# Kernel optimization log

Hardware: AMD Instinct MI355X
Metric: run time of the kernel (lower is better)

Reference implementation:

```python
import jax, jax.numpy as jnp
import numpy as np

E = 8        # n_routed_experts
K = 2        # n_experts_per_token
H = 1024     # d_hidden
D = 512      # d_expert
NSH = 2      # n_shared_experts -> shared expert width = D*NSH


def setup_inputs() -> dict:
    key = jax.random.key(0)
    ks = jax.random.split(key, 8)
    s = 0.02
    x = jax.random.normal(ks[0], (4, 2048, H), jnp.float32)
    W_router = (jax.random.normal(ks[1], (H, E), jnp.float32) * s)
    Wg = (jax.random.normal(ks[2], (E, H, D), jnp.float32) * s)   # per-expert gate proj
    Wu = (jax.random.normal(ks[3], (E, H, D), jnp.float32) * s)   # per-expert up proj
    Wd = (jax.random.normal(ks[4], (E, D, H), jnp.float32) * s)   # per-expert down proj
    Ds = D * NSH
    Wsg = (jax.random.normal(ks[5], (H, Ds), jnp.float32) * s)
    Wsu = (jax.random.normal(ks[6], (H, Ds), jnp.float32) * s)
    Wsd = (jax.random.normal(ks[7], (Ds, H), jnp.float32) * s)
    return {"x": x, "W_router": W_router, "Wg": Wg, "Wu": Wu, "Wd": Wd,
            "Wsg": Wsg, "Wsu": Wsu, "Wsd": Wsd}


def reference(x, W_router, Wg, Wu, Wd, Wsg, Wsu, Wsd):
    B, S, Hd = x.shape
    T = B * S
    xf = x.reshape(T, Hd)

    # shared expert (SwiGLU)
    shared = (jax.nn.silu(xf @ Wsg) * (xf @ Wsu)) @ Wsd          # [T, H]

    # gating: softmax -> top-k -> renormalize
    logits = xf @ W_router                                        # [T, E]
    probs = jax.nn.softmax(logits, axis=-1)
    topk_scores, topk_idx = jax.lax.top_k(probs, K)               # [T, K]
    topk_scores = topk_scores / jnp.sum(topk_scores, axis=-1, keepdims=True)

    # combine weights: zero for unselected experts (topk indices are distinct,
    # so the original's first-match score selection equals a simple scatter)
    combine = jnp.zeros((T, E), x.dtype).at[jnp.arange(T)[:, None], topk_idx].set(topk_scores)

    # per-expert SwiGLU, computed densely and combined with sparse weights
    gate = jax.nn.silu(jnp.einsum('th,ehd->etd', xf, Wg))         # [E, T, D]
    up = jnp.einsum('th,ehd->etd', xf, Wu)                        # [E, T, D]
    expert_out = jnp.einsum('etd,edh->eth', gate * up, Wd)        # [E, T, H]
    routed = jnp.einsum('eth,te->th', expert_out, combine)        # [T, H]

    out = (routed + shared).reshape(B, S, Hd)

    # load-balancing aux loss: E * sum(mean_probs^2)
    probs_mean = jnp.mean(probs.reshape(B, S, E), axis=(0, 1))
    aux_loss = E * jnp.sum(probs_mean * probs_mean)
    return out, aux_loss
```

## Files before the change

kernel.cpp:

```cpp
#include <hip/hip_runtime.h>


typedef unsigned short u16;
typedef unsigned int   u32;
typedef short short8 __attribute__((ext_vector_type(8)));
typedef float f32x4  __attribute__((ext_vector_type(4)));

#define AS1 __attribute__((address_space(1)))
#define AS3 __attribute__((address_space(3)))

constexpr int T  = 8192;
constexpr int H  = 1024;
constexpr int E  = 8;
constexpr int D  = 512;
constexpr int DS = 1024;
constexpr int PAIR_CAP  = 18432;
constexpr int MT_ROUTED = 72;
constexpr int RB = 512;

constexpr int GU_ROUTED_BLKS = 4 * MT_ROUTED;
constexpr int GU_SHARED_BLKS = 8 * (T / 256);
constexpr int DR_BLKS = 4 * MT_ROUTED;
constexpr int DSH_BLKS = 4 * (T / 256);

__device__ __forceinline__ u16 f2bf(float f){
  u32 u = __builtin_bit_cast(u32, f);
  u += 0x7fffu + ((u >> 16) & 1u);
  return (u16)(u >> 16);
}
__device__ __forceinline__ float bf2f(u16 h){
  u32 u = ((u32)h) << 16;
  return __builtin_bit_cast(float, u);
}

__device__ __forceinline__ void gl_lds16(const u16* g, u16* l){
  __builtin_amdgcn_global_load_lds((const AS1 void*)g, (AS3 void*)l, 16, 0, 0);
}

__device__ __forceinline__ void wait_vmcnt4(){ __builtin_amdgcn_s_waitcnt(0x0f74); }
__device__ __forceinline__ void wait_vmcnt0(){ __builtin_amdgcn_s_waitcnt(0x0f70); }

__device__ __forceinline__ void bar(){
  __builtin_amdgcn_s_barrier();
  __builtin_amdgcn_sched_barrier(0);
}

__device__ __forceinline__ int swz_off(int c, int lane){
  return ((c ^ (lane & 7)) * 8);
}

__global__ void __launch_bounds__(256) router_kernel(
    const float* __restrict__ x, const float* __restrict__ Wr,
    u16* __restrict__ xb,
    int* __restrict__ topk_idx, float* __restrict__ topk_w,
    int* __restrict__ partial_hist, float* __restrict__ partial_probs)
{
  __shared__ int   hist_s[4][8];
  __shared__ float ps_s[4][8];
  int tid = threadIdx.x, lane = tid & 63, wv = tid >> 6;
  int   histl[8] = {0,0,0,0,0,0,0,0};
  float psl[8]   = {0.f,0.f,0.f,0.f,0.f,0.f,0.f,0.f};

  for (int it = 0; it < 4; ++it){
    int t = blockIdx.x * 16 + wv * 4 + it;
    const float4* xr = (const float4*)(x + (long)t * H);
    uint2* xbr = (uint2*)(xb + (long)t * H);
    float acc[8];
#pragma unroll
    for (int e = 0; e < 8; ++e) acc[e] = 0.f;
#pragma unroll
    for (int i = 0; i < 4; ++i){
      float4 xv = xr[i * 64 + lane];
      u32 lo = (u32)f2bf(xv.x) | ((u32)f2bf(xv.y) << 16);
      u32 hi = (u32)f2bf(xv.z) | ((u32)f2bf(xv.w) << 16);
      xbr[i * 64 + lane] = make_uint2(lo, hi);
      int h0 = i * 256 + lane * 4;
#pragma unroll
      for (int j = 0; j < 4; ++j){
        float xs = (j == 0) ? xv.x : (j == 1) ? xv.y : (j == 2) ? xv.z : xv.w;
        const float4* wr = (const float4*)(Wr + (long)(h0 + j) * E);
        float4 w0 = wr[0], w1 = wr[1];
        acc[0] += xs * w0.x; acc[1] += xs * w0.y; acc[2] += xs * w0.z; acc[3] += xs * w0.w;
        acc[4] += xs * w1.x; acc[5] += xs * w1.y; acc[6] += xs * w1.z; acc[7] += xs * w1.w;
      }
    }
#pragma unroll
    for (int off = 32; off >= 1; off >>= 1){
#pragma unroll
      for (int e = 0; e < 8; ++e) acc[e] += __shfl_xor(acc[e], off, 64);
    }
    if (lane == 0){
      float m = acc[0];
#pragma unroll
      for (int e = 1; e < 8; ++e) m = fmaxf(m, acc[e]);
      float p[8], s = 0.f;
#pragma unroll
      for (int e = 0; e < 8; ++e){ p[e] = __expf(acc[e] - m); s += p[e]; }
      float inv = 1.f / s;
#pragma unroll
      for (int e = 0; e < 8; ++e) psl[e] += p[e] * inv;
      int i1 = 0; float v1 = p[0];
#pragma unroll
      for (int e = 1; e < 8; ++e) if (p[e] > v1){ v1 = p[e]; i1 = e; }
      int i2 = -1; float v2 = -1.f;
#pragma unroll
      for (int e = 0; e < 8; ++e) if (e != i1 && p[e] > v2){ v2 = p[e]; i2 = e; }
      float rs = 1.f / (v1 + v2);
      topk_idx[2 * t] = i1; topk_idx[2 * t + 1] = i2;
      topk_w[2 * t] = v1 * rs; topk_w[2 * t + 1] = v2 * rs;
      histl[i1]++; histl[i2]++;
    }
  }
  if (lane == 0){
#pragma unroll
    for (int e = 0; e < 8; ++e){ hist_s[wv][e] = histl[e]; ps_s[wv][e] = psl[e]; }
  }
  __syncthreads();
  if (tid < 8){
    int hs = 0; float ps = 0.f;
#pragma unroll
    for (int w = 0; w < 4; ++w){ hs += hist_s[w][tid]; ps += ps_s[w][tid]; }
    partial_hist[blockIdx.x * 8 + tid]  = hs;
    partial_probs[blockIdx.x * 8 + tid] = ps;
  }
}

__global__ void __launch_bounds__(64) scan_kernel(
    const int* __restrict__ partial_hist, const float* __restrict__ partial_probs,
    int* __restrict__ block_offset, float* __restrict__ out_aux,
    int* __restrict__ meta)
{
  __shared__ int   csum[8][8];
  __shared__ float cps[8][8];
  __shared__ int   cbase[8][8];
  __shared__ int   base_s[8];
  int tid = threadIdx.x, e = tid & 7, c = tid >> 3;
  int s = 0; float f = 0.f;
  for (int b = c * 64; b < c * 64 + 64; ++b){
    s += partial_hist[b * 8 + e]; f += partial_probs[b * 8 + e];
  }
  csum[c][e] = s; cps[c][e] = f;
  __syncthreads();
  if (tid < 8){
    int tot = 0;
    for (int cc = 0; cc < 8; ++cc){ cbase[cc][tid] = tot; tot += csum[cc][tid]; }
    csum[0][tid] = tot;
  }
  __syncthreads();
  if (tid == 0){
    int off = 0;
    for (int ee = 0; ee < 8; ++ee){ base_s[ee] = off; off += (csum[0][ee] + 255) & ~255; }
    meta[0] = off;
    float a = 0.f;
    for (int ee = 0; ee < 8; ++ee){
      float ps = 0.f;
      for (int cc = 0; cc < 8; ++cc) ps += cps[cc][ee];
      float m = ps * (1.f / (float)T);
      a += m * m;
    }
    out_aux[0] = (float)E * a;
  }
  __syncthreads();
  int run = base_s[e] + cbase[c][e];
  for (int b = c * 64; b < c * 64 + 64; ++b){
    block_offset[b * 8 + e] = run;
    run += partial_hist[b * 8 + e];
  }
}

__global__ void __launch_bounds__(64) scatter_kernel(
    const int* __restrict__ topk_idx, const float* __restrict__ topk_w,
    const int* __restrict__ block_offset,
    int* __restrict__ pair_token, int* __restrict__ pair_expert,
    float* __restrict__ pair_score, int* __restrict__ token_pos)
{
  int lane = threadIdx.x, b = blockIdx.x;
  if (lane >= 32) return;
  int idx = b * 32 + lane;
  int t = idx >> 1;
  int e = topk_idx[idx];
  float w = topk_w[idx];
  unsigned long long below = lane ? ((1ull << lane) - 1ull) : 0ull;
  int rank = 0, basee = 0;
#pragma unroll
  for (int ee = 0; ee < 8; ++ee){
    unsigned long long m = __ballot(e == ee);
    if (e == ee){ rank = __popcll(m & below); basee = block_offset[b * 8 + ee]; }
  }
  int pos = basee + rank;
  pair_token[pos] = t;
  pair_expert[pos] = e;
  pair_score[pos] = w;
  token_pos[idx] = pos;
}

__global__ void __launch_bounds__(256) transpose_all(
    const float* __restrict__ Wsg, const float* __restrict__ Wsu, u16* __restrict__ WsguT,
    const float* __restrict__ Wsd, u16* __restrict__ WsdT,
    const float* __restrict__ Wg,  const float* __restrict__ Wu, u16* __restrict__ WguT,
    const float* __restrict__ Wd,  u16* __restrict__ WdT)
{
  __shared__ float tile[32][33];
  int z = blockIdx.z;
  const float* src; u16* dst; int R, C, itype;
  if (z < 3){
    R = 1024; C = 1024;
    if (z == 0){ src = Wsg; dst = WsguT; itype = 1; }
    else if (z == 1){ src = Wsu; dst = WsguT; itype = 2; }
    else { src = Wsd; dst = WsdT; itype = 0; }
  } else if (z < 19){
    R = 1024; C = 512;
    int p = z - 3;
    if (p < 8){ src = Wg + (long)p * R * C; dst = WguT + (long)p * (2 * D * H); itype = 1; }
    else      { src = Wu + (long)(p - 8) * R * C; dst = WguT + (long)(p - 8) * (2 * D * H); itype = 2; }
  } else {
    R = 512; C = 1024;
    int p = z - 19;
    src = Wd + (long)p * R * C; dst = WdT + (long)p * R * C; itype = 0;
  }
  int tx = threadIdx.x & 31, ty = threadIdx.x >> 5;
  int c = blockIdx.x * 32 + tx;
  int rb = blockIdx.y * 32;
  if (blockIdx.x * 32 >= C || rb >= R) return;
#pragma unroll
  for (int j = 0; j < 4; ++j)
    tile[ty + j * 8][tx] = src[(long)(rb + ty + j * 8) * C + c];
  __syncthreads();
#pragma unroll
  for (int j = 0; j < 4; ++j){
    int cc = blockIdx.x * 32 + ty + j * 8;
    int dr = (itype == 0) ? cc : ((cc >> 4) * 32 + (cc & 15) + ((itype == 2) ? 16 : 0));
    dst[(long)dr * R + rb + tx] = f2bf(tile[tx][ty + j * 8]);
  }
}

struct HalfStage { const u16* p[2]; };

__device__ __forceinline__ void half_init(HalfStage& hs, const u16* __restrict__ gbase,
    int ld, int rowbase, const int* __restrict__ gather, int wave, int lane){
  int lr = lane >> 3, ch = lane & 7;
  int chs = (ch ^ lr) * 8;
#pragma unroll
  for (int j = 0; j < 2; ++j){
    int row = (wave * 2 + j) * 8 + lr;
    int grow = gather ? gather[rowbase + row] : (rowbase + row);
    hs.p[j] = gbase + (long)grow * ld + chs;
  }
}

__device__ __forceinline__ void half_issue(const HalfStage& hs, int k0,
                                           u16* __restrict__ lds, int wave){
#pragma unroll
  for (int j = 0; j < 2; ++j)
    gl_lds16(hs.p[j] + k0, lds + (wave * 2 + j) * 512);
}

template<int EPI>
__device__ __forceinline__ void gemm256(
    const u16* __restrict__ A, const u16* __restrict__ B, int K, int NT,
    const int* __restrict__ gather, int m0, int n0,
    u16* __restrict__ o_bf, int o_ld,
    const float* __restrict__ pair_score,
    const int* __restrict__ token_pos, const u16* __restrict__ rout,
    float* __restrict__ out,
    u16* __restrict__ As, u16* __restrict__ Bs)
{
  int tid = threadIdx.x, lane = tid & 63, wave = tid >> 6;
  int wm = wave >> 2, wn = wave & 3;
  int rl = lane & 15, q = lane >> 4;

  HalfStage a0, a1, b0, b1;
  half_init(a0, A, K, m0,       gather, wave, lane);
  half_init(a1, A, K, m0 + 128, gather, wave, lane);
  half_init(b0, B, K, n0,       nullptr, wave, lane);
  half_init(b1, B, K, n0 + 128, nullptr, wave, lane);

  f32x4 acc[8][4];
#pragma unroll
  for (int i = 0; i < 8; ++i)
#pragma unroll
    for (int j = 0; j < 4; ++j)
#pragma unroll
      for (int r = 0; r < 4; ++r) acc[i][j][r] = 0.f;

  half_issue(b0, 0, Bs + 0 * 8192, wave);
  half_issue(b1, 0, Bs + 1 * 8192, wave);
  half_issue(a0, 0, As + 0 * 8192, wave);
  half_issue(a1, 0, As + 1 * 8192, wave);
  if (NT > 1){
    half_issue(b0, 64, Bs + 2 * 8192, wave);
    half_issue(b1, 64, Bs + 3 * 8192, wave);
    wait_vmcnt4();
  } else {
    wait_vmcnt0();
  }
  bar();

  int bhalf = wn >> 1, brow0 = (wn & 1) * 64;

#pragma unroll 1
  for (int t = 0; t < NT; ++t){
    int buf = t & 1, nbuf = buf ^ 1;
    const u16* Abase = As + (buf * 2 + wm) * 8192;
    const u16* Bbase = Bs + (buf * 2 + bhalf) * 8192;
    short8 bfr[2][4];
#pragma unroll
    for (int qd = 0; qd < 4; ++qd){
      short8 afr[2][2];
#pragma unroll
      for (int ks = 0; ks < 2; ++ks){
        int off = swz_off(ks * 4 + q, lane);
#pragma unroll
        for (int m = 0; m < 2; ++m)
          afr[ks][m] = *(const short8*)(Abase + (qd * 32 + m * 16 + rl) * 64 + off);
        if (qd == 0){
#pragma unroll
          for (int n = 0; n < 4; ++n)
            bfr[ks][n] = *(const short8*)(Bbase + (brow0 + n * 16 + rl) * 64 + off);
        }
      }
      if (qd == 0 && t + 1 < NT) half_issue(a0, (t + 1) * 64, As + (nbuf * 2 + 0) * 8192, wave);
      if (qd == 1 && t + 1 < NT) half_issue(a1, (t + 1) * 64, As + (nbuf * 2 + 1) * 8192, wave);
      if (qd == 2 && t + 2 < NT) half_issue(b0, (t + 2) * 64, Bs + (buf * 2 + 0) * 8192, wave);
      if (qd == 3 && t + 2 < NT) half_issue(b1, (t + 2) * 64, Bs + (buf * 2 + 1) * 8192, wave);
      bar();
      __builtin_amdgcn_s_setprio(1);
#pragma unroll
      for (int ks = 0; ks < 2; ++ks)
#pragma unroll
        for (int m = 0; m < 2; ++m)
#pragma unroll
          for (int n = 0; n < 4; ++n)
            acc[qd * 2 + m][n] = __builtin_amdgcn_mfma_f32_16x16x32_bf16(
                afr[ks][m], bfr[ks][n], acc[qd * 2 + m][n], 0, 0, 0);
      __builtin_amdgcn_s_setprio(0);
      if (qd == 3){
        if (t + 2 < NT) wait_vmcnt4(); else wait_vmcnt0();
      }
      bar();
    }
  }

  int row0 = m0 + wm * 128;
  if constexpr (EPI == 0){
    int hcol0 = (n0 >> 1) + wn * 32;
#pragma unroll
    for (int mt = 0; mt < 8; ++mt)
#pragma unroll
      for (int ntp = 0; ntp < 2; ++ntp)
#pragma unroll
        for (int r = 0; r < 4; ++r){
          int row = row0 + mt * 16 + q * 4 + r;
          int col = hcol0 + ntp * 16 + rl;
          float g = acc[mt][2 * ntp][r], u = acc[mt][2 * ntp + 1][r];
          float h = g / (1.f + __expf(-g)) * u;
          o_bf[(long)row * o_ld + col] = f2bf(h);
        }
  } else if constexpr (EPI == 1){
    int col0 = n0 + wn * 64;
#pragma unroll
    for (int mt = 0; mt < 8; ++mt)
#pragma unroll
      for (int r = 0; r < 4; ++r){
        int row = row0 + mt * 16 + q * 4 + r;
        float s = pair_score[row];
        long rbase = (long)row * H;
#pragma unroll
        for (int n = 0; n < 4; ++n){
          int col = col0 + n * 16 + rl;
          o_bf[rbase + col] = f2bf(s * acc[mt][n][r]);
        }
      }
  } else {
    int col0 = n0 + wn * 64;
#pragma unroll
    for (int mt = 0; mt < 8; ++mt)
#pragma unroll
      for (int r = 0; r < 4; ++r){
        int row = row0 + mt * 16 + q * 4 + r;
        int p0 = token_pos[2 * row], p1 = token_pos[2 * row + 1];
        long o = (long)row * H;
#pragma unroll
        for (int n = 0; n < 4; ++n){
          int col = col0 + n * 16 + rl;
          out[o + col] = acc[mt][n][r]
                       + bf2f(rout[(long)p0 * H + col])
                       + bf2f(rout[(long)p1 * H + col]);
        }
      }
  }
}

__global__ void __launch_bounds__(512, 2) gateup_fused(
    const u16* __restrict__ xb, const u16* __restrict__ WguT, u16* __restrict__ hr,
    const u16* __restrict__ WsguT, u16* __restrict__ hs,
    const int* __restrict__ pair_token, const int* __restrict__ pair_expert,
    const int* __restrict__ meta)
{
  __shared__ u16 As[4 * 8192];
  __shared__ u16 Bs[4 * 8192];
  int fid = blockIdx.x;
  if (fid < GU_ROUTED_BLKS){
    int x8 = fid & 7, s = fid >> 3;
    int mtile = x8 + 8 * (s >> 2), ntile = s & 3;
    int m0 = mtile * 256;
    if (m0 >= meta[0]) return;
    int e = pair_expert[m0];
    gemm256<0>(xb, WguT + (long)e * (2 * D * H), H, H / 64, pair_token,
               m0, ntile * 256, hr, D, nullptr, nullptr, nullptr, nullptr, As, Bs);
  } else {
    int lid = fid - GU_ROUTED_BLKS;
    int x8 = lid & 7, s = lid >> 3;
    int mtile = x8 + 8 * (s >> 3), ntile = s & 7;
    gemm256<0>(xb, WsguT, H, H / 64, nullptr,
               mtile * 256, ntile * 256, hs, DS, nullptr, nullptr, nullptr, nullptr, As, Bs);
  }
}

__global__ void __launch_bounds__(512, 2) down_routed_kernel(
    const u16* __restrict__ hr, const u16* __restrict__ WdT, u16* __restrict__ rout,
    const float* __restrict__ pair_score, const int* __restrict__ pair_expert,
    const int* __restrict__ meta)
{
  __shared__ u16 As[4 * 8192];
  __shared__ u16 Bs[4 * 8192];
  int fid = blockIdx.x;
  int x8 = fid & 7, s = fid >> 3;
  int mtile = x8 + 8 * (s >> 2), ntile = s & 3;
  int m0 = mtile * 256;
  if (m0 >= meta[0]) return;
  int e = pair_expert[m0];
  gemm256<1>(hr, WdT + (long)e * (H * D), D, D / 64, nullptr,
             m0, ntile * 256, rout, H, pair_score, nullptr, nullptr, nullptr, As, Bs);
}

__global__ void __launch_bounds__(512, 2) down_shared_kernel(
    const u16* __restrict__ hs, const u16* __restrict__ WsdT,
    const u16* __restrict__ rout, const int* __restrict__ token_pos,
    float* __restrict__ out)
{
  __shared__ u16 As[4 * 8192];
  __shared__ u16 Bs[4 * 8192];
  int fid = blockIdx.x;
  int x8 = fid & 7, s = fid >> 3;
  int mtile = x8 + 8 * (s >> 2), ntile = s & 3;
  gemm256<2>(hs, WsdT, DS, DS / 64, nullptr,
             mtile * 256, ntile * 256, nullptr, 0, nullptr, token_pos, rout, out, As, Bs);
}

extern "C" void kernel_launch(void* const* d_in, const int* in_sizes, int n_in,
                              void* d_out, int out_size, void* d_ws, size_t ws_size,
                              hipStream_t stream)
{
  (void)in_sizes; (void)n_in; (void)out_size; (void)ws_size;
  const float* x   = (const float*)d_in[0];
  const float* Wr  = (const float*)d_in[1];
  const float* Wg  = (const float*)d_in[2];
  const float* Wu  = (const float*)d_in[3];
  const float* Wd  = (const float*)d_in[4];
  const float* Wsg = (const float*)d_in[5];
  const float* Wsu = (const float*)d_in[6];
  const float* Wsd = (const float*)d_in[7];
  float* out = (float*)d_out;

  char* ws = (char*)d_ws;
  size_t off = 0;
  auto alloc = [&](size_t bytes) -> void* {
    void* p = ws + off; off += (bytes + 255) & ~(size_t)255; return p;
  };
  u16* xb    = (u16*)alloc((size_t)T * H * 2);
  u16* WsguT = (u16*)alloc((size_t)2 * DS * H * 2);
  u16* WsdT  = (u16*)alloc((size_t)H * DS * 2);
  u16* WguT  = (u16*)alloc((size_t)E * 2 * D * H * 2);
  u16* WdT   = (u16*)alloc((size_t)E * H * D * 2);
  u16* hs    = (u16*)alloc((size_t)T * DS * 2);
  u16* hr    = (u16*)alloc((size_t)PAIR_CAP * D * 2);
  u16* rout  = (u16*)alloc((size_t)PAIR_CAP * H * 2);
  int*   topk_idx  = (int*)alloc((size_t)T * 2 * 4);
  float* topk_w    = (float*)alloc((size_t)T * 2 * 4);
  int*   token_pos = (int*)alloc((size_t)T * 2 * 4);
  int*   partial_hist  = (int*)alloc((size_t)RB * 8 * 4);
  float* partial_probs = (float*)alloc((size_t)RB * 8 * 4);
  int*   block_offset  = (int*)alloc((size_t)RB * 8 * 4);
  int*   meta          = (int*)alloc(256);
  char* zbase = ws + off;
  int*   pair_token  = (int*)alloc((size_t)PAIR_CAP * 4);
  int*   pair_expert = (int*)alloc((size_t)PAIR_CAP * 4);
  float* pair_score  = (float*)alloc((size_t)PAIR_CAP * 4);
  size_t zbytes = (size_t)((ws + off) - zbase);

  hipMemsetAsync(zbase, 0, zbytes, stream);

  transpose_all<<<dim3(32, 32, 27), 256, 0, stream>>>(
      Wsg, Wsu, WsguT, Wsd, WsdT, Wg, Wu, WguT, Wd, WdT);

  router_kernel<<<RB, 256, 0, stream>>>(x, Wr, xb, topk_idx, topk_w,
                                        partial_hist, partial_probs);
  scan_kernel<<<1, 64, 0, stream>>>(partial_hist, partial_probs, block_offset,
                                    out + (size_t)T * H, meta);
  scatter_kernel<<<RB, 64, 0, stream>>>(topk_idx, topk_w, block_offset,
                                        pair_token, pair_expert, pair_score, token_pos);

  gateup_fused<<<GU_ROUTED_BLKS + GU_SHARED_BLKS, 512, 0, stream>>>(
      xb, WguT, hr, WsguT, hs, pair_token, pair_expert, meta);

  down_routed_kernel<<<DR_BLKS, 512, 0, stream>>>(
      hr, WdT, rout, pair_score, pair_expert, meta);
  down_shared_kernel<<<DSH_BLKS, 512, 0, stream>>>(
      hs, WsdT, rout, token_pos, out);
}
```

Measured before the change: 364.0 us.

## Halve down-proj N tile, double block count, add XCD-aware block remapping

Templates the GEMM on the number of B halves so the down-projection kernels use 256x128 tiles instead of 256x256, doubling their grid size and halving their B LDS buffers. This targets low occupancy and wave quantization in the down-projection kernels. It also replaces the old interleaved tile mapping with an XCD-aware block index permutation in all three GEMM kernels, aiming for better L2 reuse per chiplet. A sched_barrier is also added before the s_barrier. The cost is more re-reads of the A operand because there are more N tiles.

Result: faster. 354.5 us (-2.6%).

```diff
diff --git a/kernel.cpp b/kernel.cpp
--- a/kernel.cpp
+++ b/kernel.cpp
@@ -20,8 +20,9 @@
 
 constexpr int GU_ROUTED_BLKS = 4 * MT_ROUTED;
 constexpr int GU_SHARED_BLKS = 8 * (T / 256);
-constexpr int DR_BLKS = 4 * MT_ROUTED;
-constexpr int DSH_BLKS = 4 * (T / 256);
+constexpr int GU_BLKS  = GU_ROUTED_BLKS + GU_SHARED_BLKS;
+constexpr int DR_BLKS  = 8 * MT_ROUTED;
+constexpr int DSH_BLKS = 8 * (T / 256);
 
 __device__ __forceinline__ u16 f2bf(float f){
   u32 u = __builtin_bit_cast(u32, f);
@@ -37,16 +38,22 @@
   __builtin_amdgcn_global_load_lds((const AS1 void*)g, (AS3 void*)l, 16, 0, 0);
 }
 
-__device__ __forceinline__ void wait_vmcnt4(){ __builtin_amdgcn_s_waitcnt(0x0f74); }
-__device__ __forceinline__ void wait_vmcnt0(){ __builtin_amdgcn_s_waitcnt(0x0f70); }
+template<int N>
+__device__ __forceinline__ void wait_vm(){ __builtin_amdgcn_s_waitcnt(0x0f70 | N); }
 
 __device__ __forceinline__ void bar(){
+  __builtin_amdgcn_sched_barrier(0);
   __builtin_amdgcn_s_barrier();
   __builtin_amdgcn_sched_barrier(0);
 }
 
 __device__ __forceinline__ int swz_off(int c, int lane){
   return ((c ^ (lane & 7)) * 8);
+}
+
+template<int NWG>
+__device__ __forceinline__ int xcd_tau(int fid){
+  return (fid & 7) * (NWG >> 3) + (fid >> 3);
 }
 
 __global__ void __launch_bounds__(256) router_kernel(
@@ -255,7 +262,7 @@
     gl_lds16(hs.p[j] + k0, lds + (wave * 2 + j) * 512);
 }
 
-template<int EPI>
+template<int EPI, int BH>
 __device__ __forceinline__ void gemm256(
     const u16* __restrict__ A, const u16* __restrict__ B, int K, int NT,
     const int* __restrict__ gather, int m0, int n0,
@@ -265,6 +272,7 @@
     float* __restrict__ out,
     u16* __restrict__ As, u16* __restrict__ Bs)
 {
+  constexpr int NB = 2 * BH;
   int tid = threadIdx.x, lane = tid & 63, wave = tid >> 6;
   int wm = wave >> 2, wn = wave & 3;
   int rl = lane & 15, q = lane >> 4;
@@ -273,37 +281,38 @@
   half_init(a0, A, K, m0,       gather, wave, lane);
   half_init(a1, A, K, m0 + 128, gather, wave, lane);
   half_init(b0, B, K, n0,       nullptr, wave, lane);
-  half_init(b1, B, K, n0 + 128, nullptr, wave, lane);
-
-  f32x4 acc[8][4];
+  if (BH == 2) half_init(b1, B, K, n0 + 128, nullptr, wave, lane);
+
+  f32x4 acc[8][NB];
 #pragma unroll
   for (int i = 0; i < 8; ++i)
 #pragma unroll
-    for (int j = 0; j < 4; ++j)
+    for (int j = 0; j < NB; ++j)
 #pragma unroll
       for (int r = 0; r < 4; ++r) acc[i][j][r] = 0.f;
 
   half_issue(b0, 0, Bs + 0 * 8192, wave);
-  half_issue(b1, 0, Bs + 1 * 8192, wave);
+  if (BH == 2) half_issue(b1, 0, Bs + 1 * 8192, wave);
   half_issue(a0, 0, As + 0 * 8192, wave);
   half_issue(a1, 0, As + 1 * 8192, wave);
   if (NT > 1){
-    half_issue(b0, 64, Bs + 2 * 8192, wave);
-    half_issue(b1, 64, Bs + 3 * 8192, wave);
-    wait_vmcnt4();
+    half_issue(b0, 64, Bs + (BH + 0) * 8192, wave);
+    if (BH == 2) half_issue(b1, 64, Bs + 3 * 8192, wave);
+    wait_vm<2 * BH>();
   } else {
-    wait_vmcnt0();
+    wait_vm<0>();
   }
   bar();
 
-  int bhalf = wn >> 1, brow0 = (wn & 1) * 64;
+  int bhalf = (BH == 2) ? (wn >> 1) : 0;
+  int brow0 = (BH == 2) ? (wn & 1) * 64 : wn * 32;
 
 #pragma unroll 1
   for (int t = 0; t < NT; ++t){
     int buf = t & 1, nbuf = buf ^ 1;
     const u16* Abase = As + (buf * 2 + wm) * 8192;
-    const u16* Bbase = Bs + (buf * 2 + bhalf) * 8192;
-    short8 bfr[2][4];
+    const u16* Bbase = Bs + (buf * BH + bhalf) * 8192;
+    short8 bfr[2][NB];
 #pragma unroll
     for (int qd = 0; qd < 4; ++qd){
       short8 afr[2][2];
@@ -315,14 +324,14 @@
           afr[ks][m] = *(const short8*)(Abase + (qd * 32 + m * 16 + rl) * 64 + off);
         if (qd == 0){
 #pragma unroll
-          for (int n = 0; n < 4; ++n)
+          for (int n = 0; n < NB; ++n)
             bfr[ks][n] = *(const short8*)(Bbase + (brow0 + n * 16 + rl) * 64 + off);
         }
       }
       if (qd == 0 && t + 1 < NT) half_issue(a0, (t + 1) * 64, As + (nbuf * 2 + 0) * 8192, wave);
       if (qd == 1 && t + 1 < NT) half_issue(a1, (t + 1) * 64, As + (nbuf * 2 + 1) * 8192, wave);
-      if (qd == 2 && t + 2 < NT) half_issue(b0, (t + 2) * 64, Bs + (buf * 2 + 0) * 8192, wave);
-      if (qd == 3 && t + 2 < NT) half_issue(b1, (t + 2) * 64, Bs + (buf * 2 + 1) * 8192, wave);
+      if (qd == 2 && t + 2 < NT) half_issue(b0, (t + 2) * 64, Bs + (buf * BH + 0) * 8192, wave);
+      if (BH == 2 && qd == 3 && t + 2 < NT) half_issue(b1, (t + 2) * 64, Bs + (buf * 2 + 1) * 8192, wave);
       bar();
       __builtin_amdgcn_s_setprio(1);
 #pragma unroll
@@ -330,12 +339,12 @@
 #pragma unroll
         for (int m = 0; m < 2; ++m)
 #pragma unroll
-          for (int n = 0; n < 4; ++n)
+          for (int n = 0; n < NB; ++n)
             acc[qd * 2 + m][n] = __builtin_amdgcn_mfma_f32_16x16x32_bf16(
                 afr[ks][m], bfr[ks][n], acc[qd * 2 + m][n], 0, 0, 0);
       __builtin_amdgcn_s_setprio(0);
       if (qd == 3){
-        if (t + 2 < NT) wait_vmcnt4(); else wait_vmcnt0();
+        if (t + 2 < NT) wait_vm<2 * BH>(); else wait_vm<0>();
       }
       bar();
     }
@@ -357,7 +366,7 @@
           o_bf[(long)row * o_ld + col] = f2bf(h);
         }
   } else if constexpr (EPI == 1){
-    int col0 = n0 + wn * 64;
+    int col0 = n0 + wn * (16 * NB);
 #pragma unroll
     for (int mt = 0; mt < 8; ++mt)
 #pragma unroll
@@ -366,13 +375,13 @@
         float s = pair_score[row];
         long rbase = (long)row * H;
 #pragma unroll
-        for (int n = 0; n < 4; ++n){
+        for (int n = 0; n < NB; ++n){
           int col = col0 + n * 16 + rl;
           o_bf[rbase + col] = f2bf(s * acc[mt][n][r]);
         }
       }
   } else {
-    int col0 = n0 + wn * 64;
+    int col0 = n0 + wn * (16 * NB);
 #pragma unroll
     for (int mt = 0; mt < 8; ++mt)
 #pragma unroll
@@ -381,7 +390,7 @@
         int p0 = token_pos[2 * row], p1 = token_pos[2 * row + 1];
         long o = (long)row * H;
 #pragma unroll
-        for (int n = 0; n < 4; ++n){
+        for (int n = 0; n < NB; ++n){
           int col = col0 + n * 16 + rl;
           out[o + col] = acc[mt][n][r]
                        + bf2f(rout[(long)p0 * H + col])
@@ -399,21 +408,19 @@
 {
   __shared__ u16 As[4 * 8192];
   __shared__ u16 Bs[4 * 8192];
-  int fid = blockIdx.x;
-  if (fid < GU_ROUTED_BLKS){
-    int x8 = fid & 7, s = fid >> 3;
-    int mtile = x8 + 8 * (s >> 2), ntile = s & 3;
+  int tau = xcd_tau<GU_BLKS>(blockIdx.x);
+  if (tau < GU_ROUTED_BLKS){
+    int mtile = tau >> 2, ntile = tau & 3;
     int m0 = mtile * 256;
     if (m0 >= meta[0]) return;
     int e = pair_expert[m0];
-    gemm256<0>(xb, WguT + (long)e * (2 * D * H), H, H / 64, pair_token,
-               m0, ntile * 256, hr, D, nullptr, nullptr, nullptr, nullptr, As, Bs);
+    gemm256<0, 2>(xb, WguT + (long)e * (2 * D * H), H, H / 64, pair_token,
+                  m0, ntile * 256, hr, D, nullptr, nullptr, nullptr, nullptr, As, Bs);
   } else {
-    int lid = fid - GU_ROUTED_BLKS;
-    int x8 = lid & 7, s = lid >> 3;
-    int mtile = x8 + 8 * (s >> 3), ntile = s & 7;
-    gemm256<0>(xb, WsguT, H, H / 64, nullptr,
-               mtile * 256, ntile * 256, hs, DS, nullptr, nullptr, nullptr, nullptr, As, Bs);
+    int sidx = tau - GU_ROUTED_BLKS;
+    int mtile = sidx >> 3, ntile = sidx & 7;
+    gemm256<0, 2>(xb, WsguT, H, H / 64, nullptr,
+                  mtile * 256, ntile * 256, hs, DS, nullptr, nullptr, nullptr, nullptr, As, Bs);
   }
 }
 
@@ -423,15 +430,14 @@
     const int* __restrict__ meta)
 {
   __shared__ u16 As[4 * 8192];
-  __shared__ u16 Bs[4 * 8192];
-  int fid = blockIdx.x;
-  int x8 = fid & 7, s = fid >> 3;
-  int mtile = x8 + 8 * (s >> 2), ntile = s & 3;
+  __shared__ u16 Bs[2 * 8192];
+  int tau = xcd_tau<DR_BLKS>(blockIdx.x);
+  int mtile = tau >> 3, ntile = tau & 7;
   int m0 = mtile * 256;
   if (m0 >= meta[0]) return;
   int e = pair_expert[m0];
-  gemm256<1>(hr, WdT + (long)e * (H * D), D, D / 64, nullptr,
-             m0, ntile * 256, rout, H, pair_score, nullptr, nullptr, nullptr, As, Bs);
+  gemm256<1, 1>(hr, WdT + (long)e * (H * D), D, D / 64, nullptr,
+                m0, ntile * 128, rout, H, pair_score, nullptr, nullptr, nullptr, As, Bs);
 }
 
 __global__ void __launch_bounds__(512, 2) down_shared_kernel(
@@ -440,12 +446,11 @@
     float* __restrict__ out)
 {
   __shared__ u16 As[4 * 8192];
-  __shared__ u16 Bs[4 * 8192];
-  int fid = blockIdx.x;
-  int x8 = fid & 7, s = fid >> 3;
-  int mtile = x8 + 8 * (s >> 2), ntile = s & 3;
-  gemm256<2>(hs, WsdT, DS, DS / 64, nullptr,
-             mtile * 256, ntile * 256, nullptr, 0, nullptr, token_pos, rout, out, As, Bs);
+  __shared__ u16 Bs[2 * 8192];
+  int tau = xcd_tau<DSH_BLKS>(blockIdx.x);
+  int mtile = tau >> 3, ntile = tau & 7;
+  gemm256<2, 1>(hs, WsdT, DS, DS / 64, nullptr,
+                mtile * 256, ntile * 128, nullptr, 0, nullptr, token_pos, rout, out, As, Bs);
 }
 
 extern "C" void kernel_launch(void* const* d_in, const int* in_sizes, int n_in,
@@ -501,7 +506,7 @@
   scatter_kernel<<<RB, 64, 0, stream>>>(topk_idx, topk_w, block_offset,
                                         pair_token, pair_expert, pair_score, token_pos);
 
-  gateup_fused<<<GU_ROUTED_BLKS + GU_SHARED_BLKS, 512, 0, stream>>>(
+  gateup_fused<<<GU_BLKS, 512, 0, stream>>>(
       xb, WguT, hr, WsguT, hs, pair_token, pair_expert, meta);
 
   down_routed_kernel<<<DR_BLKS, 512, 0, stream>>>(
```

## Fuse routed and shared down GEMMs, split combine into kernel, add XCD remap

Applied to the files above, without the earlier changes.

Runs the routed and shared down-projection GEMMs in a single launch, so the shared GEMM no longer waits for the routed one and the two can run at the same time. The gather-add of the routed outputs moves out of the shared GEMM epilogue into a separate lightweight combine kernel that reads back the fp32 output. Block indices in both GEMM launches are remapped so that consecutive tiles land on the same XCD. A sched_barrier is also added before s_barrier. The cost is an extra launch and an extra read-modify-write pass over the fp32 output.

New measurement: 367.9 us. No clear change (+1.1%).

```diff
diff --git a/kernel.cpp b/kernel.cpp
--- a/kernel.cpp
+++ b/kernel.cpp
@@ -20,8 +20,10 @@
 
 constexpr int GU_ROUTED_BLKS = 4 * MT_ROUTED;
 constexpr int GU_SHARED_BLKS = 8 * (T / 256);
-constexpr int DR_BLKS = 4 * MT_ROUTED;
-constexpr int DSH_BLKS = 4 * (T / 256);
+constexpr int GU_BLKS  = GU_ROUTED_BLKS + GU_SHARED_BLKS;
+constexpr int DNR_BLKS = 4 * MT_ROUTED;
+constexpr int DNS_BLKS = 4 * (T / 256);
+constexpr int DN_BLKS  = DNR_BLKS + DNS_BLKS;
 
 __device__ __forceinline__ u16 f2bf(float f){
   u32 u = __builtin_bit_cast(u32, f);
@@ -37,16 +39,22 @@
   __builtin_amdgcn_global_load_lds((const AS1 void*)g, (AS3 void*)l, 16, 0, 0);
 }
 
-__device__ __forceinline__ void wait_vmcnt4(){ __builtin_amdgcn_s_waitcnt(0x0f74); }
-__device__ __forceinline__ void wait_vmcnt0(){ __builtin_amdgcn_s_waitcnt(0x0f70); }
+template<int N>
+__device__ __forceinline__ void wait_vm(){ __builtin_amdgcn_s_waitcnt(0x0f70 | N); }
 
 __device__ __forceinline__ void bar(){
+  __builtin_amdgcn_sched_barrier(0);
   __builtin_amdgcn_s_barrier();
   __builtin_amdgcn_sched_barrier(0);
 }
 
 __device__ __forceinline__ int swz_off(int c, int lane){
   return ((c ^ (lane & 7)) * 8);
+}
+
+template<int NWG>
+__device__ __forceinline__ int xcd_tau(int fid){
+  return (fid & 7) * (NWG >> 3) + (fid >> 3);
 }
 
 __global__ void __launch_bounds__(256) router_kernel(
@@ -260,9 +268,7 @@
     const u16* __restrict__ A, const u16* __restrict__ B, int K, int NT,
     const int* __restrict__ gather, int m0, int n0,
     u16* __restrict__ o_bf, int o_ld,
-    const float* __restrict__ pair_score,
-    const int* __restrict__ token_pos, const u16* __restrict__ rout,
-    float* __restrict__ out,
+    const float* __restrict__ pair_score, float* __restrict__ out,
     u16* __restrict__ As, u16* __restrict__ Bs)
 {
   int tid = threadIdx.x, lane = tid & 63, wave = tid >> 6;
@@ -290,9 +296,9 @@
   if (NT > 1){
     half_issue(b0, 64, Bs + 2 * 8192, wave);
     half_issue(b1, 64, Bs + 3 * 8192, wave);
-    wait_vmcnt4();
+    wait_vm<4>();
   } else {
-    wait_vmcnt0();
+    wait_vm<0>();
   }
   bar();
 
@@ -335,7 +341,7 @@
                 afr[ks][m], bfr[ks][n], acc[qd * 2 + m][n], 0, 0, 0);
       __builtin_amdgcn_s_setprio(0);
       if (qd == 3){
-        if (t + 2 < NT) wait_vmcnt4(); else wait_vmcnt0();
+        if (t + 2 < NT) wait_vm<4>(); else wait_vm<0>();
       }
       bar();
     }
@@ -378,14 +384,11 @@
 #pragma unroll
       for (int r = 0; r < 4; ++r){
         int row = row0 + mt * 16 + q * 4 + r;
-        int p0 = token_pos[2 * row], p1 = token_pos[2 * row + 1];
         long o = (long)row * H;
 #pragma unroll
         for (int n = 0; n < 4; ++n){
           int col = col0 + n * 16 + rl;
-          out[o + col] = acc[mt][n][r]
-                       + bf2f(rout[(long)p0 * H + col])
-                       + bf2f(rout[(long)p1 * H + col]);
+          out[o + col] = acc[mt][n][r];
         }
       }
   }
@@ -399,53 +402,70 @@
 {
   __shared__ u16 As[4 * 8192];
   __shared__ u16 Bs[4 * 8192];
-  int fid = blockIdx.x;
-  if (fid < GU_ROUTED_BLKS){
-    int x8 = fid & 7, s = fid >> 3;
-    int mtile = x8 + 8 * (s >> 2), ntile = s & 3;
+  int tau = xcd_tau<GU_BLKS>(blockIdx.x);
+  if (tau < GU_ROUTED_BLKS){
+    int mtile = tau >> 2, ntile = tau & 3;
     int m0 = mtile * 256;
     if (m0 >= meta[0]) return;
     int e = pair_expert[m0];
     gemm256<0>(xb, WguT + (long)e * (2 * D * H), H, H / 64, pair_token,
-               m0, ntile * 256, hr, D, nullptr, nullptr, nullptr, nullptr, As, Bs);
+               m0, ntile * 256, hr, D, nullptr, nullptr, As, Bs);
   } else {
-    int lid = fid - GU_ROUTED_BLKS;
-    int x8 = lid & 7, s = lid >> 3;
-    int mtile = x8 + 8 * (s >> 3), ntile = s & 7;
+    int sidx = tau - GU_ROUTED_BLKS;
+    int mtile = sidx >> 3, ntile = sidx & 7;
     gemm256<0>(xb, WsguT, H, H / 64, nullptr,
-               mtile * 256, ntile * 256, hs, DS, nullptr, nullptr, nullptr, nullptr, As, Bs);
-  }
-}
-
-__global__ void __launch_bounds__(512, 2) down_routed_kernel(
+               mtile * 256, ntile * 256, hs, DS, nullptr, nullptr, As, Bs);
+  }
+}
+
+__global__ void __launch_bounds__(512, 2) down_fused(
     const u16* __restrict__ hr, const u16* __restrict__ WdT, u16* __restrict__ rout,
     const float* __restrict__ pair_score, const int* __restrict__ pair_expert,
-    const int* __restrict__ meta)
+    const int* __restrict__ meta,
+    const u16* __restrict__ hs, const u16* __restrict__ WsdT,
+    float* __restrict__ out)
 {
   __shared__ u16 As[4 * 8192];
   __shared__ u16 Bs[4 * 8192];
-  int fid = blockIdx.x;
-  int x8 = fid & 7, s = fid >> 3;
-  int mtile = x8 + 8 * (s >> 2), ntile = s & 3;
-  int m0 = mtile * 256;
-  if (m0 >= meta[0]) return;
-  int e = pair_expert[m0];
-  gemm256<1>(hr, WdT + (long)e * (H * D), D, D / 64, nullptr,
-             m0, ntile * 256, rout, H, pair_score, nullptr, nullptr, nullptr, As, Bs);
-}
-
-__global__ void __launch_bounds__(512, 2) down_shared_kernel(
-    const u16* __restrict__ hs, const u16* __restrict__ WsdT,
-    const u16* __restrict__ rout, const int* __restrict__ token_pos,
-    float* __restrict__ out)
-{
-  __shared__ u16 As[4 * 8192];
-  __shared__ u16 Bs[4 * 8192];
-  int fid = blockIdx.x;
-  int x8 = fid & 7, s = fid >> 3;
-  int mtile = x8 + 8 * (s >> 2), ntile = s & 3;
-  gemm256<2>(hs, WsdT, DS, DS / 64, nullptr,
-             mtile * 256, ntile * 256, nullptr, 0, nullptr, token_pos, rout, out, As, Bs);
+  int tau = xcd_tau<DN_BLKS>(blockIdx.x);
+  if (tau < DNR_BLKS){
+    int mtile = tau >> 2, ntile = tau & 3;
+    int m0 = mtile * 256;
+    if (m0 >= meta[0]) return;
+    int e = pair_expert[m0];
+    gemm256<1>(hr, WdT + (long)e * (H * D), D, D / 64, nullptr,
+               m0, ntile * 256, rout, H, pair_score, nullptr, As, Bs);
+  } else {
+    int sidx = tau - DNR_BLKS;
+    int mtile = sidx >> 2, ntile = sidx & 3;
+    gemm256<2>(hs, WsdT, DS, DS / 64, nullptr,
+               mtile * 256, ntile * 256, nullptr, 0, nullptr, out, As, Bs);
+  }
+}
+
+__global__ void __launch_bounds__(256) combine_kernel(
+    float* __restrict__ out, const u16* __restrict__ rout,
+    const int* __restrict__ token_pos)
+{
+  int tid = threadIdx.x, lane = tid & 63, wv = tid >> 6;
+#pragma unroll
+  for (int it = 0; it < 4; ++it){
+    int t = blockIdx.x * 16 + wv * 4 + it;
+    int p0 = token_pos[2 * t], p1 = token_pos[2 * t + 1];
+    const uint2* r0 = (const uint2*)(rout + (long)p0 * H);
+    const uint2* r1 = (const uint2*)(rout + (long)p1 * H);
+    float4* o = (float4*)(out + (long)t * H);
+#pragma unroll
+    for (int i = 0; i < 4; ++i){
+      uint2 a = r0[i * 64 + lane], b = r1[i * 64 + lane];
+      float4 v = o[i * 64 + lane];
+      v.x += bf2f((u16)(a.x & 0xffff)) + bf2f((u16)(b.x & 0xffff));
+      v.y += bf2f((u16)(a.x >> 16))    + bf2f((u16)(b.x >> 16));
+      v.z += bf2f((u16)(a.y & 0xffff)) + bf2f((u16)(b.y & 0xffff));
+      v.w += bf2f((u16)(a.y >> 16))    + bf2f((u16)(b.y >> 16));
+      o[i * 64 + lane] = v;
+    }
+  }
 }
 
 extern "C" void kernel_launch(void* const* d_in, const int* in_sizes, int n_in,
@@ -501,11 +521,11 @@
   scatter_kernel<<<RB, 64, 0, stream>>>(topk_idx, topk_w, block_offset,
                                         pair_token, pair_expert, pair_score, token_pos);
 
-  gateup_fused<<<GU_ROUTED_BLKS + GU_SHARED_BLKS, 512, 0, stream>>>(
+  gateup_fused<<<GU_BLKS, 512, 0, stream>>>(
       xb, WguT, hr, WsguT, hs, pair_token, pair_expert, meta);
 
-  down_routed_kernel<<<DR_BLKS, 512, 0, stream>>>(
-      hr, WdT, rout, pair_score, pair_expert, meta);
-  down_shared_kernel<<<DSH_BLKS, 512, 0, stream>>>(
-      hs, WsdT, rout, token_pos, out);
-}
+  down_fused<<<DN_BLKS, 512, 0, stream>>>(
+      hr, WdT, rout, pair_score, pair_expert, meta, hs, WsdT, out);
+
+  combine_kernel<<<T / 16, 256, 0, stream>>>(out, rout, token_pos);
+}
```
